# Optimization experiments

Measured on AMD Instinct MI355X. Metric: run time of the kernel, lower is better.

## Reference

```python
import jax, jax.numpy as jnp
import numpy as np

B, T, C = 4, 2048, 1024
H = 16
HS = C // H

def setup_inputs() -> dict:
    key = jax.random.key(0)
    ks = jax.random.split(key, 5)
    s = 0.02
    return {
        "x": jax.random.normal(ks[0], (B, T, C), dtype=jnp.float32),
        "c_attn_w": jax.random.normal(ks[1], (C, 3 * C), dtype=jnp.float32) * s,
        "c_attn_b": jax.random.normal(ks[2], (3 * C,), dtype=jnp.float32) * s,
        "c_proj_w": jax.random.normal(ks[3], (C, C), dtype=jnp.float32) * s,
        "c_proj_b": jax.random.normal(ks[4], (C,), dtype=jnp.float32) * s,
    }

def reference(x, c_attn_w, c_attn_b, c_proj_w, c_proj_b):
    b, t, c = x.shape
    qkv = x @ c_attn_w + c_attn_b                       # (B,T,3C)
    q, k, v = jnp.split(qkv, 3, axis=2)
    # (B,T,C) -> (B,H,T,hs)
    q = q.reshape(b, t, H, HS).transpose(0, 2, 1, 3)
    k = k.reshape(b, t, H, HS).transpose(0, 2, 1, 3)
    v = v.reshape(b, t, H, HS).transpose(0, 2, 1, 3)
    scale = 1.0 / np.sqrt(HS).astype(np.float32)
    attn = jnp.einsum("bhqd,bhkd->bhqk", q, k) * scale  # (B,H,T,T)
    causal = jnp.tril(jnp.ones((t, t), dtype=bool))
    attn = jnp.where(causal[None, None, :, :], attn, -jnp.inf)
    attn = jax.nn.softmax(attn, axis=-1)
    y = jnp.einsum("bhqk,bhkd->bhqd", attn, v)          # (B,H,T,hs)
    y = y.transpose(0, 2, 1, 3).reshape(b, t, c)        # (B,T,C)
    return y @ c_proj_w + c_proj_b
```

## Files before the change

kernel.cpp:

```cpp
#include <hip/hip_runtime.h>

typedef __attribute__((ext_vector_type(8))) _Float16 h8;
typedef __attribute__((ext_vector_type(4))) _Float16 h4;
typedef __attribute__((ext_vector_type(4))) float f4;
typedef __attribute__((ext_vector_type(16))) float f16x;
typedef __attribute__((ext_vector_type(4))) unsigned u4;

#define MFMA16(a,b,c) __builtin_amdgcn_mfma_f32_16x16x32_f16(a,b,c,0,0,0)
#define MFMA32(a,b,c) __builtin_amdgcn_mfma_f32_32x32x16_f16(a,b,c,0,0,0)

__device__ inline void gload16(const void* g, void* l) {
    __builtin_amdgcn_global_load_lds(
        (const __attribute__((address_space(1))) void*)g,
        (__attribute__((address_space(3))) void*)l, 16, 0, 0);
}

__device__ inline float swap_half(float x) { return __shfl_xor(x, 32, 64); }

__global__ __launch_bounds__(256) void k_f32_to_f16(const float* __restrict__ in,
                                                    _Float16* __restrict__ out, int n4) {
    int i = blockIdx.x * 256 + threadIdx.x;
    if (i < n4) {
        float4 v = ((const float4*)in)[i];
        h4 h;
        h[0] = (_Float16)v.x; h[1] = (_Float16)v.y;
        h[2] = (_Float16)v.z; h[3] = (_Float16)v.w;
        ((h4*)out)[i] = h;
    }
}

__global__ __launch_bounds__(256) void k_transpose_f16(const float* __restrict__ W,
                                                       _Float16* __restrict__ Wt,
                                                       int K, int N) {
    __shared__ float tile[64 * 68];
    const int k0 = blockIdx.x * 64, n0 = blockIdx.y * 64;
    const int t = threadIdx.x;
    const int tr = t >> 4;
    const int tc = t & 15;
#pragma unroll
    for (int i = 0; i < 4; ++i) {
        int r = tr + i * 16;
        float4 v = *(const float4*)(W + (size_t)(k0 + r) * N + n0 + tc * 4);
        *(float4*)(&tile[r * 68 + tc * 4]) = v;
    }
    __syncthreads();
#pragma unroll
    for (int i = 0; i < 4; ++i) {
        int nl = tr + i * 16;
        h4 hv;
#pragma unroll
        for (int j = 0; j < 4; ++j)
            hv[j] = (_Float16)tile[(tc * 4 + j) * 68 + nl];
        *(h4*)(Wt + (size_t)(n0 + nl) * K + k0 + tc * 4) = hv;
    }
}

template <int MODE>
__global__ __launch_bounds__(256) void k_gemm(const _Float16* __restrict__ A,
                                              const _Float16* __restrict__ Bt,
                                              const float* __restrict__ bias,
                                              _Float16* __restrict__ oQ,
                                              _Float16* __restrict__ oK,
                                              _Float16* __restrict__ oV,
                                              float* __restrict__ oF,
                                              int M, int N, int K) {
    __shared__ _Float16 As[2][128 * 32];
    __shared__ _Float16 Bs[2][128 * 32];
    const int tid = threadIdx.x;
    const int lane = tid & 63, wv = tid >> 6;
    const int wm = wv >> 1, wn = wv & 1;
    const int l15 = lane & 15, l4 = lane >> 4;
    const int bm = blockIdx.x * 128, bn = blockIdx.y * 128;
    f4 acc[4][4] = {};

    const int srow = lane >> 2, scol = (lane & 3) * 8;
    const _Float16* Ag = A + (size_t)(bm + srow) * K + scol;
    const _Float16* Bg = Bt + (size_t)(bn + srow) * K + scol;

#pragma unroll
    for (int j = 0; j < 2; ++j) {
        const int rb_ = (wv * 2 + j) * 16;
        gload16(Ag + (size_t)rb_ * K, &As[0][(wv * 2 + j) * 512]);
        gload16(Bg + (size_t)rb_ * K, &Bs[0][(wv * 2 + j) * 512]);
    }
    asm volatile("s_waitcnt vmcnt(0)" ::: "memory");
    __syncthreads();

    int cur = 0;
    for (int k0 = 0; k0 < K; k0 += 32) {
        if (k0 + 32 < K) {
#pragma unroll
            for (int j = 0; j < 2; ++j) {
                const int rb_ = (wv * 2 + j) * 16;
                gload16(Ag + (size_t)rb_ * K + k0 + 32, &As[cur ^ 1][(wv * 2 + j) * 512]);
                gload16(Bg + (size_t)rb_ * K + k0 + 32, &Bs[cur ^ 1][(wv * 2 + j) * 512]);
            }
        }

        const _Float16* Ac = As[cur];
        const _Float16* Bc = Bs[cur];
        h8 af[4], bf[4];
#pragma unroll
        for (int i = 0; i < 4; ++i)
            af[i] = *(const h8*)(&Ac[(wm * 64 + i * 16 + l15) * 32 + l4 * 8]);
#pragma unroll
        for (int i = 0; i < 4; ++i)
            bf[i] = *(const h8*)(&Bc[(wn * 64 + i * 16 + l15) * 32 + l4 * 8]);
        __builtin_amdgcn_s_setprio(1);
#pragma unroll
        for (int mi = 0; mi < 4; ++mi)
#pragma unroll
            for (int ni = 0; ni < 4; ++ni)
                acc[mi][ni] = MFMA16(af[mi], bf[ni], acc[mi][ni]);
        __builtin_amdgcn_s_setprio(0);

        asm volatile("s_waitcnt vmcnt(0)" ::: "memory");
        __syncthreads();
        cur ^= 1;
    }

#pragma unroll
    for (int mi = 0; mi < 4; ++mi) {
#pragma unroll
        for (int ni = 0; ni < 4; ++ni) {
            int col = bn + wn * 64 + ni * 16 + l15;
            float bv = bias[col];
            int rb = bm + wm * 64 + mi * 16 + l4 * 4;
            if (MODE == 0) {
                int which = col >> 10, n1 = col & 1023;
                int hh = n1 >> 6, dd = n1 & 63;
                if (which == 2) {
                    int b = rb >> 11, tq = rb & 2047;
                    h4 pv;
#pragma unroll
                    for (int i = 0; i < 4; ++i) pv[i] = (_Float16)(acc[mi][ni][i] + bv);
                    *(h4*)(oV + ((size_t)(b * 16 + hh) * 64 + dd) * 2048 + tq) = pv;
                } else {
                    _Float16* dst = which == 0 ? oQ : oK;
                    const float scl = which == 0 ? 0.18033688011112042f : 1.0f;
#pragma unroll
                    for (int i = 0; i < 4; ++i) {
                        int row = rb + i;
                        int b = row >> 11, tq = row & 2047;
                        dst[(((size_t)b * 16 + hh) * 2048 + tq) * 64 + dd] =
                            (_Float16)((acc[mi][ni][i] + bv) * scl);
                    }
                }
            } else {
#pragma unroll
                for (int i = 0; i < 4; ++i)
                    oF[(size_t)(rb + i) * N + col] = acc[mi][ni][i] + bv;
            }
        }
    }
}

#define SWZI(row, cb) ((((row) << 7) + ((cb) ^ ((((row) & 7) << 4)))) >> 1)

__global__ __launch_bounds__(256) void k_attn(const _Float16* __restrict__ Qh,
                                              const _Float16* __restrict__ Kh,
                                              const _Float16* __restrict__ Vt,
                                              _Float16* __restrict__ Yh) {
    __shared__ _Float16 lds[8192];
    const int bid = blockIdx.x;
    const int bh = bid & 63;
    const int qt = 15 - (bid >> 6);
    const int tid = threadIdx.x, w = tid >> 6;
    const int l31 = tid & 31, hi = (tid >> 5) & 1;
    const int h16 = hi * 16, h4o = hi * 4;
    const size_t base = (size_t)bh * 2048 * 64;

    const int qabs = qt * 128 + w * 32 + l31;
    h8 qf[4];
#pragma unroll
    for (int dk = 0; dk < 4; ++dk)
        qf[dk] = *(const h8*)(Qh + base + (size_t)qabs * 64 + dk * 16 + hi * 8);

    f16x O0 = {}, O1 = {};
    float m = -1e30f, l = 0.f;

    const int sr = tid >> 3;
    const int sc8 = (tid & 7) * 8;
    const int scb = (tid & 7) * 16;
    const int kbb = 2 * qt + 1;
    const int kbw = 2 * qt + (w >> 1);

    {
#pragma unroll
        for (int j = 0; j < 2; ++j) {
            int row = j * 32 + sr;
            h8 kv = *(const h8*)(Kh + base + (size_t)row * 64 + sc8);
            h8 vv = *(const h8*)(Vt + base + (size_t)row * 2048 + sc8);
            *(h8*)(&lds[SWZI(row, scb)]) = kv;
            *(h8*)(&lds[4096 + SWZI(row, scb)]) = vv;
        }
    }
    __syncthreads();

    for (int kb = 0; kb <= kbb; ++kb) {
        const bool pre = (kb < kbb);
        h8 kn[2], vn[2];
        if (pre) {
#pragma unroll
            for (int j = 0; j < 2; ++j) {
                int row = j * 32 + sr;
                kn[j] = *(const h8*)(Kh + base + (size_t)((kb + 1) * 64 + row) * 64 + sc8);
                vn[j] = *(const h8*)(Vt + base + (size_t)row * 2048 + (kb + 1) * 64 + sc8);
            }
        }

        if (kb <= kbw) {
            f16x S0 = {}, S1 = {};
            __builtin_amdgcn_s_setprio(1);
#pragma unroll
            for (int dk = 0; dk < 4; ++dk) {
                h8 kf0 = *(const h8*)(&lds[SWZI(l31, dk * 32 + h16)]);
                h8 kf1 = *(const h8*)(&lds[SWZI(32 + l31, dk * 32 + h16)]);
                S0 = MFMA32(kf0, qf[dk], S0);
                S1 = MFMA32(kf1, qf[dk], S1);
            }
            __builtin_amdgcn_s_setprio(0);

            if (kb == kbw) {
#pragma unroll
                for (int r = 0; r < 16; ++r) {
                    int key = kb * 64 + (r & 3) + 8 * (r >> 2) + h4o;
                    if (key > qabs) S0[r] = -1e30f;
                    if (key + 32 > qabs) S1[r] = -1e30f;
                }
            }

            float tr[16];
#pragma unroll
            for (int r = 0; r < 16; ++r) tr[r] = fmaxf(S0[r], S1[r]);
#pragma unroll
            for (int st = 8; st >= 1; st >>= 1)
#pragma unroll
                for (int r = 0; r < st; ++r) tr[r] = fmaxf(tr[r], tr[r + st]);
            float pm = fmaxf(tr[0], swap_half(tr[0]));
            if (!__all(pm - m <= 8.f)) {
                float mnew = fmaxf(m, pm);
                float scl = __builtin_amdgcn_exp2f(m - mnew);
                m = mnew;
                l *= scl;
#pragma unroll
                for (int r = 0; r < 16; ++r) { O0[r] *= scl; O1[r] *= scl; }
            }
#pragma unroll
            for (int r = 0; r < 16; ++r) {
                S0[r] = __builtin_amdgcn_exp2f(S0[r] - m);
                S1[r] = __builtin_amdgcn_exp2f(S1[r] - m);
            }
#pragma unroll
            for (int r = 0; r < 16; ++r) tr[r] = S0[r] + S1[r];
#pragma unroll
            for (int st = 8; st >= 1; st >>= 1)
#pragma unroll
                for (int r = 0; r < st; ++r) tr[r] += tr[r + st];
            l += tr[0] + swap_half(tr[0]);

            h8 pb[4];
#pragma unroll
            for (int kk = 0; kk < 4; ++kk) {
                const int bb = (kk & 1) * 8;
                unsigned W0, W1, W2, W3;
                if (kk < 2) {
                    W0 = __builtin_bit_cast(unsigned, __builtin_amdgcn_cvt_pkrtz(S0[bb + 0], S0[bb + 1]));
                    W1 = __builtin_bit_cast(unsigned, __builtin_amdgcn_cvt_pkrtz(S0[bb + 2], S0[bb + 3]));
                    W2 = __builtin_bit_cast(unsigned, __builtin_amdgcn_cvt_pkrtz(S0[bb + 4], S0[bb + 5]));
                    W3 = __builtin_bit_cast(unsigned, __builtin_amdgcn_cvt_pkrtz(S0[bb + 6], S0[bb + 7]));
                } else {
                    W0 = __builtin_bit_cast(unsigned, __builtin_amdgcn_cvt_pkrtz(S1[bb + 0], S1[bb + 1]));
                    W1 = __builtin_bit_cast(unsigned, __builtin_amdgcn_cvt_pkrtz(S1[bb + 2], S1[bb + 3]));
                    W2 = __builtin_bit_cast(unsigned, __builtin_amdgcn_cvt_pkrtz(S1[bb + 4], S1[bb + 5]));
                    W3 = __builtin_bit_cast(unsigned, __builtin_amdgcn_cvt_pkrtz(S1[bb + 6], S1[bb + 7]));
                }
                unsigned E0 = (unsigned)__shfl_xor((int)(hi ? W0 : W2), 32, 64);
                unsigned E1 = (unsigned)__shfl_xor((int)(hi ? W1 : W3), 32, 64);
                u4 wvv;
                wvv[0] = hi ? E0 : W0;
                wvv[1] = hi ? E1 : W1;
                wvv[2] = hi ? W2 : E0;
                wvv[3] = hi ? W3 : E1;
                pb[kk] = __builtin_bit_cast(h8, wvv);
            }

            __builtin_amdgcn_s_setprio(1);
#pragma unroll
            for (int kk = 0; kk < 4; ++kk) {
                h8 vf0 = *(const h8*)(&lds[4096 + SWZI(l31, kk * 32 + h16)]);
                h8 vf1 = *(const h8*)(&lds[4096 + SWZI(32 + l31, kk * 32 + h16)]);
                O0 = MFMA32(vf0, pb[kk], O0);
                O1 = MFMA32(vf1, pb[kk], O1);
            }
            __builtin_amdgcn_s_setprio(0);
        }

        __syncthreads();
        if (pre) {
#pragma unroll
            for (int j = 0; j < 2; ++j) {
                int row = j * 32 + sr;
                *(h8*)(&lds[SWZI(row, scb)]) = kn[j];
                *(h8*)(&lds[4096 + SWZI(row, scb)]) = vn[j];
            }
            __syncthreads();
        }
    }

    __syncthreads();

    {
        float inv = 1.0f / l;
        const int R = w * 32 + l31;
#pragma unroll
        for (int rr = 0; rr < 4; ++rr) {
            h4 a, b;
#pragma unroll
            for (int q = 0; q < 4; ++q) {
                a[q] = (_Float16)(O0[rr * 4 + q] * inv);
                b[q] = (_Float16)(O1[rr * 4 + q] * inv);
            }
            *(h4*)(&lds[SWZI(R, rr * 16 + hi * 8)]) = a;
            *(h4*)(&lds[SWZI(R, 64 + rr * 16 + hi * 8)]) = b;
        }
    }
    __syncthreads();
    {
        const int b = bh >> 4, head = bh & 15;
        const int row = tid >> 1;
#pragma unroll
        for (int i = 0; i < 4; ++i) {
            int seg = (tid & 1) * 4 + i;
            h8 v = *(const h8*)(&lds[SWZI(row, seg * 16)]);
            *(h8*)(Yh + ((size_t)(b * 2048 + qt * 128 + row)) * 1024 + head * 64 + seg * 8) = v;
        }
    }
}

extern "C" void kernel_launch(void* const* d_in, const int* in_sizes, int n_in,
                              void* d_out, int out_size, void* d_ws, size_t ws_size,
                              hipStream_t stream) {
    const float* x  = (const float*)d_in[0];
    const float* Wa = (const float*)d_in[1];
    const float* ba = (const float*)d_in[2];
    const float* Wp = (const float*)d_in[3];
    const float* bp = (const float*)d_in[4];
    float* out = (float*)d_out;

    _Float16* ws = (_Float16*)d_ws;
    const size_t SZ_X = (size_t)8192 * 1024;
    const size_t SZ_WA = (size_t)3072 * 1024;
    const size_t SZ_WP = (size_t)1024 * 1024;
    const size_t SZ_H = (size_t)64 * 2048 * 64;
    _Float16* xh  = ws;
    _Float16* WaT = xh + SZ_X;
    _Float16* WpT = WaT + SZ_WA;
    _Float16* Qh  = WpT + SZ_WP;
    _Float16* Kh  = Qh + SZ_H;
    _Float16* Vth = Kh + SZ_H;
    _Float16* Yh  = Vth + SZ_H;

    k_f32_to_f16<<<8192, 256, 0, stream>>>(x, xh, (int)(SZ_X / 4));
    k_transpose_f16<<<dim3(16, 48), 256, 0, stream>>>(Wa, WaT, 1024, 3072);
    k_transpose_f16<<<dim3(16, 16), 256, 0, stream>>>(Wp, WpT, 1024, 1024);
    k_gemm<0><<<dim3(64, 24), 256, 0, stream>>>(xh, WaT, ba, Qh, Kh, Vth, nullptr,
                                                8192, 3072, 1024);
    k_attn<<<1024, 256, 0, stream>>>(Qh, Kh, Vth, Yh);
    k_gemm<1><<<dim3(64, 8), 256, 0, stream>>>(Yh, WpT, bp, nullptr, nullptr, nullptr,
                                               out, 8192, 1024, 1024);
}
```

Baseline: 181.5 us.

## Rewrite GEMMs with 256xBN tiles, 512 threads, XOR-swizzled LDS and XCD remapping

```diff
diff --git a/kernel.cpp b/kernel.cpp
--- a/kernel.cpp
+++ b/kernel.cpp
@@ -55,101 +55,126 @@
     }
 }
 
-template <int MODE>
-__global__ __launch_bounds__(256) void k_gemm(const _Float16* __restrict__ A,
-                                              const _Float16* __restrict__ Bt,
-                                              const float* __restrict__ bias,
-                                              _Float16* __restrict__ oQ,
-                                              _Float16* __restrict__ oK,
-                                              _Float16* __restrict__ oV,
-                                              float* __restrict__ oF,
-                                              int M, int N, int K) {
-    __shared__ _Float16 As[2][128 * 32];
-    __shared__ _Float16 Bs[2][128 * 32];
-    const int tid = threadIdx.x;
-    const int lane = tid & 63, wv = tid >> 6;
-    const int wm = wv >> 1, wn = wv & 1;
+template <int BN, int MODE>
+__global__ __launch_bounds__(512, 2) void k_gemm2(const _Float16* __restrict__ A,
+                                                  const _Float16* __restrict__ Bt,
+                                                  const float* __restrict__ bias,
+                                                  _Float16* __restrict__ oQ,
+                                                  _Float16* __restrict__ oK,
+                                                  _Float16* __restrict__ oV,
+                                                  float* __restrict__ oF,
+                                                  int K, int N, int nbn) {
+    constexpr int NF = BN / 64;
+    __shared__ _Float16 As[2][256 * 64];
+    __shared__ _Float16 Bs[2][BN * 64];
+    const int nwg = gridDim.x;
+    const int q8 = nwg >> 3;
+    const int wg = (blockIdx.x & 7) * q8 + (blockIdx.x >> 3);
+    const int bm = (wg / nbn) * 256, bn = (wg % nbn) * BN;
+    const int tid = threadIdx.x, lane = tid & 63, wv = tid >> 6;
+    const int wm = wv >> 2, wn = wv & 3;
     const int l15 = lane & 15, l4 = lane >> 4;
-    const int bm = blockIdx.x * 128, bn = blockIdx.y * 128;
-    f4 acc[4][4] = {};
-
-    const int srow = lane >> 2, scol = (lane & 3) * 8;
-    const _Float16* Ag = A + (size_t)(bm + srow) * K + scol;
-    const _Float16* Bg = Bt + (size_t)(bn + srow) * K + scol;
-
-#pragma unroll
-    for (int j = 0; j < 2; ++j) {
-        const int rb_ = (wv * 2 + j) * 16;
-        gload16(Ag + (size_t)rb_ * K, &As[0][(wv * 2 + j) * 512]);
-        gload16(Bg + (size_t)rb_ * K, &Bs[0][(wv * 2 + j) * 512]);
-    }
+    const int sr8 = lane >> 3;
+    const int sseg = ((lane & 7) ^ sr8) * 8;
+    const _Float16* Ag = A + (size_t)(bm + wv * 8 + sr8) * K + sseg;
+    const _Float16* Bg = Bt + (size_t)(bn + wv * 8 + sr8) * K + sseg;
+    f4 acc[8][NF] = {};
+
+    const int NT = K >> 6;
+
+#pragma unroll
+    for (int j = 0; j < 4; ++j) gload16(Ag + (size_t)j * 64 * K, &As[0][(j * 64 + wv * 8) * 64]);
+#pragma unroll
+    for (int j = 0; j < NF; ++j) gload16(Bg + (size_t)j * 64 * K, &Bs[0][(j * 64 + wv * 8) * 64]);
     asm volatile("s_waitcnt vmcnt(0)" ::: "memory");
-    __syncthreads();
-
-    int cur = 0;
-    for (int k0 = 0; k0 < K; k0 += 32) {
-        if (k0 + 32 < K) {
-#pragma unroll
-            for (int j = 0; j < 2; ++j) {
-                const int rb_ = (wv * 2 + j) * 16;
-                gload16(Ag + (size_t)rb_ * K + k0 + 32, &As[cur ^ 1][(wv * 2 + j) * 512]);
-                gload16(Bg + (size_t)rb_ * K + k0 + 32, &Bs[cur ^ 1][(wv * 2 + j) * 512]);
-            }
-        }
-
-        const _Float16* Ac = As[cur];
-        const _Float16* Bc = Bs[cur];
-        h8 af[4], bf[4];
-#pragma unroll
-        for (int i = 0; i < 4; ++i)
-            af[i] = *(const h8*)(&Ac[(wm * 64 + i * 16 + l15) * 32 + l4 * 8]);
-#pragma unroll
-        for (int i = 0; i < 4; ++i)
-            bf[i] = *(const h8*)(&Bc[(wn * 64 + i * 16 + l15) * 32 + l4 * 8]);
-        __builtin_amdgcn_s_setprio(1);
-#pragma unroll
-        for (int mi = 0; mi < 4; ++mi)
-#pragma unroll
-            for (int ni = 0; ni < 4; ++ni)
-                acc[mi][ni] = MFMA16(af[mi], bf[ni], acc[mi][ni]);
-        __builtin_amdgcn_s_setprio(0);
-
-        asm volatile("s_waitcnt vmcnt(0)" ::: "memory");
-        __syncthreads();
-        cur ^= 1;
-    }
-
-#pragma unroll
-    for (int mi = 0; mi < 4; ++mi) {
-#pragma unroll
-        for (int ni = 0; ni < 4; ++ni) {
-            int col = bn + wn * 64 + ni * 16 + l15;
-            float bv = bias[col];
-            int rb = bm + wm * 64 + mi * 16 + l4 * 4;
+    __builtin_amdgcn_s_barrier();
+
+    for (int tau = 0; tau < NT; ++tau) {
+        const int s = tau & 1;
+        const bool pre = (tau + 1 < NT);
+        const size_t ko = (size_t)(tau + 1) << 6;
+
+        h8 bf[NF][2];
+#pragma unroll
+        for (int nf = 0; nf < NF; ++nf)
+#pragma unroll
+            for (int ks = 0; ks < 2; ++ks) {
+                const int row = wn * (BN / 4) + nf * 16 + l15;
+                const int seg = (ks * 4 + l4) ^ (l15 & 7);
+                bf[nf][ks] = *(const h8*)(&Bs[s][row * 64 + seg * 8]);
+            }
+
+#pragma unroll
+        for (int q = 0; q < 4; ++q) {
+            h8 af[2][2];
+#pragma unroll
+            for (int mi = 0; mi < 2; ++mi)
+#pragma unroll
+                for (int ks = 0; ks < 2; ++ks) {
+                    const int row = wm * 128 + (2 * q + mi) * 16 + l15;
+                    const int seg = (ks * 4 + l4) ^ (l15 & 7);
+                    af[mi][ks] = *(const h8*)(&As[s][row * 64 + seg * 8]);
+                }
+            if (pre) {
+                if (q == 0) {
+                    gload16(Ag + ko, &As[s ^ 1][(wv * 8) * 64]);
+                    gload16(Ag + (size_t)64 * K + ko, &As[s ^ 1][(64 + wv * 8) * 64]);
+                } else if (q == 1) {
+                    gload16(Ag + (size_t)128 * K + ko, &As[s ^ 1][(128 + wv * 8) * 64]);
+                    gload16(Ag + (size_t)192 * K + ko, &As[s ^ 1][(192 + wv * 8) * 64]);
+                } else if (q == 2) {
+#pragma unroll
+                    for (int j = 0; j < NF; ++j)
+                        gload16(Bg + (size_t)j * 64 * K + ko, &Bs[s ^ 1][(j * 64 + wv * 8) * 64]);
+                } else {
+                    asm volatile("s_waitcnt vmcnt(0)" ::: "memory");
+                }
+            }
+            __builtin_amdgcn_s_barrier();
+            __builtin_amdgcn_s_setprio(1);
+#pragma unroll
+            for (int mi = 0; mi < 2; ++mi)
+#pragma unroll
+                for (int nf = 0; nf < NF; ++nf)
+#pragma unroll
+                    for (int ks = 0; ks < 2; ++ks)
+                        acc[2 * q + mi][nf] = MFMA16(af[mi][ks], bf[nf][ks], acc[2 * q + mi][nf]);
+            __builtin_amdgcn_s_setprio(0);
+            __builtin_amdgcn_s_barrier();
+        }
+    }
+
+#pragma unroll
+    for (int mf = 0; mf < 8; ++mf) {
+#pragma unroll
+        for (int nf = 0; nf < NF; ++nf) {
+            const int col = bn + wn * (BN / 4) + nf * 16 + l15;
+            const float bv = bias[col];
+            const int rb = bm + wm * 128 + mf * 16 + l4 * 4;
             if (MODE == 0) {
-                int which = col >> 10, n1 = col & 1023;
-                int hh = n1 >> 6, dd = n1 & 63;
+                const int which = col >> 10;
+                const int hh = (col & 1023) >> 6, dd = col & 63;
                 if (which == 2) {
-                    int b = rb >> 11, tq = rb & 2047;
+                    const int b = rb >> 11, tq = rb & 2047;
                     h4 pv;
 #pragma unroll
-                    for (int i = 0; i < 4; ++i) pv[i] = (_Float16)(acc[mi][ni][i] + bv);
+                    for (int i = 0; i < 4; ++i) pv[i] = (_Float16)(acc[mf][nf][i] + bv);
                     *(h4*)(oV + ((size_t)(b * 16 + hh) * 64 + dd) * 2048 + tq) = pv;
                 } else {
                     _Float16* dst = which == 0 ? oQ : oK;
                     const float scl = which == 0 ? 0.18033688011112042f : 1.0f;
 #pragma unroll
                     for (int i = 0; i < 4; ++i) {
-                        int row = rb + i;
-                        int b = row >> 11, tq = row & 2047;
+                        const int row = rb + i;
+                        const int b = row >> 11, tq = row & 2047;
                         dst[(((size_t)b * 16 + hh) * 2048 + tq) * 64 + dd] =
-                            (_Float16)((acc[mi][ni][i] + bv) * scl);
+                            (_Float16)((acc[mf][nf][i] + bv) * scl);
                     }
                 }
             } else {
 #pragma unroll
                 for (int i = 0; i < 4; ++i)
-                    oF[(size_t)(rb + i) * N + col] = acc[mi][ni][i] + bv;
+                    oF[(size_t)(rb + i) * N + col] = acc[mf][nf][i] + bv;
             }
         }
     }
@@ -364,9 +389,9 @@
     k_f32_to_f16<<<8192, 256, 0, stream>>>(x, xh, (int)(SZ_X / 4));
     k_transpose_f16<<<dim3(16, 48), 256, 0, stream>>>(Wa, WaT, 1024, 3072);
     k_transpose_f16<<<dim3(16, 16), 256, 0, stream>>>(Wp, WpT, 1024, 1024);
-    k_gemm<0><<<dim3(64, 24), 256, 0, stream>>>(xh, WaT, ba, Qh, Kh, Vth, nullptr,
-                                                8192, 3072, 1024);
+    k_gemm2<192, 0><<<512, 512, 0, stream>>>(xh, WaT, ba, Qh, Kh, Vth, nullptr,
+                                             1024, 3072, 16);
     k_attn<<<1024, 256, 0, stream>>>(Qh, Kh, Vth, Yh);
-    k_gemm<1><<<dim3(64, 8), 256, 0, stream>>>(Yh, WpT, bp, nullptr, nullptr, nullptr,
-                                               out, 8192, 1024, 1024);
-}
+    k_gemm2<128, 1><<<256, 512, 0, stream>>>(Yh, WpT, bp, nullptr, nullptr, nullptr,
+                                             out, 1024, 1024, 8);
+}
```

Measured after the change: 181.9 us. Within noise of the previous version (+0.2%).

## Replace LDS-tiled GEMM with single-wave direct-load GEMM and XCD-aware block remap

Applied to the files above, without the earlier changes.

```diff
diff --git a/kernel.cpp b/kernel.cpp
--- a/kernel.cpp
+++ b/kernel.cpp
@@ -8,12 +8,6 @@
 
 #define MFMA16(a,b,c) __builtin_amdgcn_mfma_f32_16x16x32_f16(a,b,c,0,0,0)
 #define MFMA32(a,b,c) __builtin_amdgcn_mfma_f32_32x32x16_f16(a,b,c,0,0,0)
-
-__device__ inline void gload16(const void* g, void* l) {
-    __builtin_amdgcn_global_load_lds(
-        (const __attribute__((address_space(1))) void*)g,
-        (__attribute__((address_space(3))) void*)l, 16, 0, 0);
-}
 
 __device__ inline float swap_half(float x) { return __shfl_xor(x, 32, 64); }
 
@@ -55,57 +49,44 @@
     }
 }
 
+#define LOADAB(DA, DB, OFF)                                         \
+    DA[0] = *(const h8*)(Ap + (OFF));                               \
+    DA[1] = *(const h8*)(Ap + sA + (OFF));                          \
+    DA[2] = *(const h8*)(Ap + 2 * sA + (OFF));                      \
+    DA[3] = *(const h8*)(Ap + 3 * sA + (OFF));                      \
+    DB[0] = *(const h8*)(Bp + (OFF));                               \
+    DB[1] = *(const h8*)(Bp + sA + (OFF));                          \
+    DB[2] = *(const h8*)(Bp + 2 * sA + (OFF));                      \
+    DB[3] = *(const h8*)(Bp + 3 * sA + (OFF));
+
 template <int MODE>
-__global__ __launch_bounds__(256) void k_gemm(const _Float16* __restrict__ A,
+__global__ __launch_bounds__(64) void k_gemmD(const _Float16* __restrict__ A,
                                               const _Float16* __restrict__ Bt,
                                               const float* __restrict__ bias,
                                               _Float16* __restrict__ oQ,
                                               _Float16* __restrict__ oK,
                                               _Float16* __restrict__ oV,
                                               float* __restrict__ oF,
-                                              int M, int N, int K) {
-    __shared__ _Float16 As[2][128 * 32];
-    __shared__ _Float16 Bs[2][128 * 32];
-    const int tid = threadIdx.x;
-    const int lane = tid & 63, wv = tid >> 6;
-    const int wm = wv >> 1, wn = wv & 1;
+                                              int K, int N, int nbn) {
+    const int nwg = gridDim.x;
+    const int q8 = nwg >> 3;
+    const int wg = (blockIdx.x & 7) * q8 + (blockIdx.x >> 3);
+    const int bm = (wg / nbn) * 64, bn = (wg % nbn) * 64;
+    const int lane = threadIdx.x & 63;
     const int l15 = lane & 15, l4 = lane >> 4;
-    const int bm = blockIdx.x * 128, bn = blockIdx.y * 128;
+    const size_t sA = (size_t)16 * K;
+
+    const _Float16* Ap = A + (size_t)(bm + l15) * K + l4 * 8;
+    const _Float16* Bp = Bt + (size_t)(bn + l15) * K + l4 * 8;
+
     f4 acc[4][4] = {};
-
-    const int srow = lane >> 2, scol = (lane & 3) * 8;
-    const _Float16* Ag = A + (size_t)(bm + srow) * K + scol;
-    const _Float16* Bg = Bt + (size_t)(bn + srow) * K + scol;
-
-#pragma unroll
-    for (int j = 0; j < 2; ++j) {
-        const int rb_ = (wv * 2 + j) * 16;
-        gload16(Ag + (size_t)rb_ * K, &As[0][(wv * 2 + j) * 512]);
-        gload16(Bg + (size_t)rb_ * K, &Bs[0][(wv * 2 + j) * 512]);
-    }
-    asm volatile("s_waitcnt vmcnt(0)" ::: "memory");
-    __syncthreads();
-
-    int cur = 0;
-    for (int k0 = 0; k0 < K; k0 += 32) {
-        if (k0 + 32 < K) {
-#pragma unroll
-            for (int j = 0; j < 2; ++j) {
-                const int rb_ = (wv * 2 + j) * 16;
-                gload16(Ag + (size_t)rb_ * K + k0 + 32, &As[cur ^ 1][(wv * 2 + j) * 512]);
-                gload16(Bg + (size_t)rb_ * K + k0 + 32, &Bs[cur ^ 1][(wv * 2 + j) * 512]);
-            }
-        }
-
-        const _Float16* Ac = As[cur];
-        const _Float16* Bc = Bs[cur];
-        h8 af[4], bf[4];
-#pragma unroll
-        for (int i = 0; i < 4; ++i)
-            af[i] = *(const h8*)(&Ac[(wm * 64 + i * 16 + l15) * 32 + l4 * 8]);
-#pragma unroll
-        for (int i = 0; i < 4; ++i)
-            bf[i] = *(const h8*)(&Bc[(wn * 64 + i * 16 + l15) * 32 + l4 * 8]);
+    h8 af[4], bf[4], ag[4], bg[4];
+
+    LOADAB(af, bf, 0)
+    const int NK = K >> 5;
+    for (int kk = 0; kk < NK; kk += 2) {
+        const bool p1 = (kk + 1 < NK), p2 = (kk + 2 < NK);
+        if (p1) { LOADAB(ag, bg, 32) }
         __builtin_amdgcn_s_setprio(1);
 #pragma unroll
         for (int mi = 0; mi < 4; ++mi)
@@ -113,24 +94,31 @@
             for (int ni = 0; ni < 4; ++ni)
                 acc[mi][ni] = MFMA16(af[mi], bf[ni], acc[mi][ni]);
         __builtin_amdgcn_s_setprio(0);
-
-        asm volatile("s_waitcnt vmcnt(0)" ::: "memory");
-        __syncthreads();
-        cur ^= 1;
+        if (p2) { LOADAB(af, bf, 64) }
+        if (p1) {
+            __builtin_amdgcn_s_setprio(1);
+#pragma unroll
+            for (int mi = 0; mi < 4; ++mi)
+#pragma unroll
+                for (int ni = 0; ni < 4; ++ni)
+                    acc[mi][ni] = MFMA16(ag[mi], bg[ni], acc[mi][ni]);
+            __builtin_amdgcn_s_setprio(0);
+        }
+        Ap += 64; Bp += 64;
     }
 
 #pragma unroll
     for (int mi = 0; mi < 4; ++mi) {
 #pragma unroll
         for (int ni = 0; ni < 4; ++ni) {
-            int col = bn + wn * 64 + ni * 16 + l15;
-            float bv = bias[col];
-            int rb = bm + wm * 64 + mi * 16 + l4 * 4;
+            const int col = bn + ni * 16 + l15;
+            const float bv = bias[col];
+            const int rb = bm + mi * 16 + l4 * 4;
             if (MODE == 0) {
-                int which = col >> 10, n1 = col & 1023;
-                int hh = n1 >> 6, dd = n1 & 63;
+                const int which = col >> 10, n1 = col & 1023;
+                const int hh = n1 >> 6, dd = n1 & 63;
                 if (which == 2) {
-                    int b = rb >> 11, tq = rb & 2047;
+                    const int b = rb >> 11, tq = rb & 2047;
                     h4 pv;
 #pragma unroll
                     for (int i = 0; i < 4; ++i) pv[i] = (_Float16)(acc[mi][ni][i] + bv);
@@ -140,8 +128,8 @@
                     const float scl = which == 0 ? 0.18033688011112042f : 1.0f;
 #pragma unroll
                     for (int i = 0; i < 4; ++i) {
-                        int row = rb + i;
-                        int b = row >> 11, tq = row & 2047;
+                        const int row = rb + i;
+                        const int b = row >> 11, tq = row & 2047;
                         dst[(((size_t)b * 16 + hh) * 2048 + tq) * 64 + dd] =
                             (_Float16)((acc[mi][ni][i] + bv) * scl);
                     }
@@ -364,9 +352,9 @@
     k_f32_to_f16<<<8192, 256, 0, stream>>>(x, xh, (int)(SZ_X / 4));
     k_transpose_f16<<<dim3(16, 48), 256, 0, stream>>>(Wa, WaT, 1024, 3072);
     k_transpose_f16<<<dim3(16, 16), 256, 0, stream>>>(Wp, WpT, 1024, 1024);
-    k_gemm<0><<<dim3(64, 24), 256, 0, stream>>>(xh, WaT, ba, Qh, Kh, Vth, nullptr,
-                                                8192, 3072, 1024);
+    k_gemmD<0><<<6144, 64, 0, stream>>>(xh, WaT, ba, Qh, Kh, Vth, nullptr,
+                                        1024, 3072, 48);
     k_attn<<<1024, 256, 0, stream>>>(Qh, Kh, Vth, Yh);
-    k_gemm<1><<<dim3(64, 8), 256, 0, stream>>>(Yh, WpT, bp, nullptr, nullptr, nullptr,
-                                               out, 8192, 1024, 1024);
-}
+    k_gemmD<1><<<2048, 64, 0, stream>>>(Yh, WpT, bp, nullptr, nullptr, nullptr,
+                                        out, 1024, 1024, 16);
+}
```

After: 328.1 us. +80.8%, slower.
